# Kernel optimization log

Hardware: AMD Instinct MI355X
Metric: run time of the kernel (lower is better)

## Reference

```python
import jax, jax.numpy as jnp
import numpy as np

EMB, KEY, HEAD, CTX = 1024, 64, 64, 4096
B, T = 4, 4096

def setup_inputs() -> dict:
    key = jax.random.key(0)
    ks = jax.random.split(key, 4)
    s = 1.0 / np.sqrt(EMB)
    return {
        "embeddings": jax.random.normal(ks[0], (B, T, EMB), dtype=jnp.float32),
        "Wk": jax.random.normal(ks[1], (EMB, KEY), dtype=jnp.float32) * s,
        "bk": jnp.zeros((KEY,), dtype=jnp.float32),
        "Wq": jax.random.normal(ks[2], (EMB, KEY), dtype=jnp.float32) * s,
        "bq": jnp.zeros((KEY,), dtype=jnp.float32),
        "Wv": jax.random.normal(ks[3], (EMB, HEAD), dtype=jnp.float32) * s,
        "bv": jnp.zeros((HEAD,), dtype=jnp.float32),
    }

def reference(embeddings, Wk, bk, Wq, bq, Wv, bv):
    # Linear projections: [B, T, E] @ [E, D] -> [B, T, D]
    keys = embeddings @ Wk + bk
    queries = embeddings @ Wq + bq
    values = embeddings @ Wv + bv
    # Scores: [B, T, T]
    scores = jnp.einsum("btd,bsd->bts", queries, keys) / jnp.sqrt(jnp.float32(KEY))
    t = scores.shape[1]
    # causal mask: -inf strictly above diagonal
    causal = jnp.tril(jnp.ones((t, t), dtype=bool))
    scores = jnp.where(causal, scores, -jnp.inf)
    weights = jax.nn.softmax(scores, axis=-1)
    return jnp.einsum("bts,bsh->bth", weights, values)
```

## Files before the change

kernel.cpp:

```cpp
#include <hip/hip_runtime.h>
#include <hip/hip_bf16.h>

#define EMB 1024
#define NB  4
#define TT  4096
#define DD  64

static constexpr float SCALE2 = 0.125f * 1.4426950408889634f;

typedef __bf16          bfrag    __attribute__((ext_vector_type(8)));
typedef float           f32x4    __attribute__((ext_vector_type(4)));
typedef unsigned short  ushort8t __attribute__((ext_vector_type(8)));
typedef unsigned short  ushort4t __attribute__((ext_vector_type(4)));
typedef unsigned int    uint32;
typedef uint32          uint32x4 __attribute__((ext_vector_type(4)));

__device__ __forceinline__ unsigned short f2bf(float f) {
    __hip_bfloat16 h = __float2bfloat16(f);
    return __builtin_bit_cast(unsigned short, h);
}
__device__ __forceinline__ float bf2f(unsigned short u) {
    uint32 v = ((uint32)u) << 16;
    return __builtin_bit_cast(float, v);
}
__device__ __forceinline__ uint32 pk2(float a, float b) {
    return (uint32)f2bf(a) | ((uint32)f2bf(b) << 16);
}

__global__ __launch_bounds__(256) void prep_wt(
    const float* __restrict__ Wk, const float* __restrict__ Wq,
    const float* __restrict__ Wv, unsigned short* __restrict__ Wt)
{
    const int o = blockIdx.x * 256 + threadIdx.x;
    const int n = o >> 10, k = o & 1023;
    float v;
    if (n < 64)       v = Wk[k * 64 + n];
    else if (n < 128) v = Wq[k * 64 + (n - 64)] * SCALE2;
    else              v = Wv[k * 64 + (n - 128)];
    Wt[o] = f2bf(v);
}

#define PSTR 66

__global__ __launch_bounds__(256) void qkv_mfma(
    const float* __restrict__ emb,
    const unsigned short* __restrict__ Wt,
    const float* __restrict__ bk, const float* __restrict__ bq,
    const float* __restrict__ bv,
    unsigned short* __restrict__ Qb, unsigned short* __restrict__ Kb,
    unsigned short* __restrict__ Vt)
{
    __shared__ unsigned short elds[64 * PSTR];
    __shared__ unsigned short wlds[192 * PSTR];

    const int tid = threadIdx.x;
    const int w = tid >> 6, l = tid & 63;
    const int lr = l & 15, lg = l >> 4;
    const int m0 = blockIdx.x * 64;

    f32x4 acc[12];
#pragma unroll
    for (int i = 0; i < 12; ++i) acc[i] = (f32x4){0.f, 0.f, 0.f, 0.f};

    const int er = tid >> 2, ec = (tid & 3) * 16;

    float4 f0, f1, f2, f3;
    ushort8t wr[6];
    {
        const float* src = emb + (size_t)(m0 + er) * EMB + ec;
        f0 = *(const float4*)(src + 0);
        f1 = *(const float4*)(src + 4);
        f2 = *(const float4*)(src + 8);
        f3 = *(const float4*)(src + 12);
#pragma unroll
        for (int i = 0; i < 6; ++i) {
            const int idx = tid + i * 256;
            const int row = idx >> 3, c = (idx & 7) * 8;
            wr[i] = *(const ushort8t*)&Wt[(size_t)row * 1024 + c];
        }
    }

    for (int it = 0; it < 16; ++it) {
        __syncthreads();
        {
            ushort8t lo, hi;
            lo[0]=f2bf(f0.x); lo[1]=f2bf(f0.y); lo[2]=f2bf(f0.z); lo[3]=f2bf(f0.w);
            lo[4]=f2bf(f1.x); lo[5]=f2bf(f1.y); lo[6]=f2bf(f1.z); lo[7]=f2bf(f1.w);
            hi[0]=f2bf(f2.x); hi[1]=f2bf(f2.y); hi[2]=f2bf(f2.z); hi[3]=f2bf(f2.w);
            hi[4]=f2bf(f3.x); hi[5]=f2bf(f3.y); hi[6]=f2bf(f3.z); hi[7]=f2bf(f3.w);
            *(ushort8t*)&elds[er * PSTR + ec]     = lo;
            *(ushort8t*)&elds[er * PSTR + ec + 8] = hi;
#pragma unroll
            for (int i = 0; i < 6; ++i) {
                const int idx = tid + i * 256;
                const int row = idx >> 3, c = (idx & 7) * 8;
                *(ushort8t*)&wlds[row * PSTR + c] = wr[i];
            }
        }
        if (it < 15) {
            const int kn = (it + 1) * 64;
            const float* src = emb + (size_t)(m0 + er) * EMB + kn + ec;
            f0 = *(const float4*)(src + 0);
            f1 = *(const float4*)(src + 4);
            f2 = *(const float4*)(src + 8);
            f3 = *(const float4*)(src + 12);
#pragma unroll
            for (int i = 0; i < 6; ++i) {
                const int idx = tid + i * 256;
                const int row = idx >> 3, c = (idx & 7) * 8;
                wr[i] = *(const ushort8t*)&Wt[(size_t)row * 1024 + kn + c];
            }
        }
        __syncthreads();
#pragma unroll
        for (int c = 0; c < 2; ++c) {
            bfrag a = *(const bfrag*)&elds[(w * 16 + lr) * PSTR + c * 32 + lg * 8];
#pragma unroll
            for (int nt = 0; nt < 12; ++nt) {
                bfrag bb = *(const bfrag*)&wlds[(nt * 16 + lr) * PSTR + c * 32 + lg * 8];
                acc[nt] = __builtin_amdgcn_mfma_f32_16x16x32_bf16(a, bb, acc[nt], 0, 0, 0);
            }
        }
    }

    const int rbase = m0 + w * 16 + lg * 4;
#pragma unroll
    for (int nt = 0; nt < 12; ++nt) {
        const int n = nt * 16 + lr;
        float bias;
        if (n < 64)       bias = bk[n];
        else if (n < 128) bias = bq[n - 64] * SCALE2;
        else              bias = bv[n - 128];
        if (nt < 8) {
            unsigned short* dst = (nt < 4) ? Kb : Qb;
            const int d = (nt < 4) ? n : (n - 64);
#pragma unroll
            for (int rg = 0; rg < 4; ++rg)
                dst[(size_t)(rbase + rg) * 64 + d] = f2bf(acc[nt][rg] + bias);
        } else {
            const int h = n - 128;
            const int b = rbase >> 12, t = rbase & (TT - 1);
            ushort4t pk;
#pragma unroll
            for (int rg = 0; rg < 4; ++rg) pk[rg] = f2bf(acc[nt][rg] + bias);
            *(ushort4t*)&Vt[((size_t)b * 64 + h) * TT + t] = pk;
        }
    }
}

#define LOADK(KF, T)                                                          \
    { const unsigned short* p_ = kp0 + (size_t)(T) * 4096;                    \
      KF[0][0] = *(const bfrag*)(p_);         KF[0][1] = *(const bfrag*)(p_ + 32);   \
      KF[1][0] = *(const bfrag*)(p_ + 1024);  KF[1][1] = *(const bfrag*)(p_ + 1056); \
      KF[2][0] = *(const bfrag*)(p_ + 2048);  KF[2][1] = *(const bfrag*)(p_ + 2080); \
      KF[3][0] = *(const bfrag*)(p_ + 3072);  KF[3][1] = *(const bfrag*)(p_ + 3104); }

#define LOADV(VF, T)                                                          \
    { const unsigned short* p_ = vp0 + (T) * 64;                              \
      VF[0][0] = *(const bfrag*)(p_);             VF[0][1] = *(const bfrag*)(p_ + 32);           \
      VF[1][0] = *(const bfrag*)(p_ + 16 * TT);   VF[1][1] = *(const bfrag*)(p_ + 16 * TT + 32); \
      VF[2][0] = *(const bfrag*)(p_ + 32 * TT);   VF[2][1] = *(const bfrag*)(p_ + 32 * TT + 32); \
      VF[3][0] = *(const bfrag*)(p_ + 48 * TT);   VF[3][1] = *(const bfrag*)(p_ + 48 * TT + 32); }

#define COMPUTE(KF, VF, T)                                                    \
{                                                                             \
    const int  kt_   = kt0 + (T);                                             \
    const bool diag_ = (kt_ == nkt - 1);                                      \
    const int  k0_   = kt_ * 64;                                              \
    _Pragma("unroll")                                                         \
    for (int s = 0; s < 2; ++s) {                                             \
        f32x4 sv[4];                                                          \
        __builtin_amdgcn_s_setprio(1);                                        \
        _Pragma("unroll")                                                     \
        for (int nt = 0; nt < 4; ++nt) {                                      \
            sv[nt] = (f32x4){0.f, 0.f, 0.f, 0.f};                             \
            sv[nt] = __builtin_amdgcn_mfma_f32_16x16x32_bf16(KF[nt][0], qa[s][0], sv[nt], 0, 0, 0); \
            sv[nt] = __builtin_amdgcn_mfma_f32_16x16x32_bf16(KF[nt][1], qa[s][1], sv[nt], 0, 0, 0); \
        }                                                                     \
        __builtin_amdgcn_s_setprio(0);                                        \
        const int qrow_ = q0 + s * 16 + lr;                                   \
        if (diag_) {                                                          \
            _Pragma("unroll")                                                 \
            for (int nt = 0; nt < 4; ++nt)                                    \
                _Pragma("unroll")                                             \
                for (int rg = 0; rg < 4; ++rg) {                              \
                    const int key_ = k0_ + nt * 16 + 4 * g + rg;              \
                    if (key_ > qrow_) sv[nt][rg] = -1e30f;                    \
                }                                                             \
        }                                                                     \
        float pm = fmaxf(fmaxf(fmaxf(sv[0][0], sv[0][1]), fmaxf(sv[0][2], sv[0][3])),   \
                         fmaxf(fmaxf(sv[1][0], sv[1][1]), fmaxf(sv[1][2], sv[1][3])));  \
        pm = fmaxf(pm, fmaxf(fmaxf(fmaxf(sv[2][0], sv[2][1]), fmaxf(sv[2][2], sv[2][3])),   \
                             fmaxf(fmaxf(sv[3][0], sv[3][1]), fmaxf(sv[3][2], sv[3][3])))); \
        pm = fmaxf(pm, __shfl_xor(pm, 16));                                   \
        pm = fmaxf(pm, __shfl_xor(pm, 32));                                   \
        if (!__all(pm - mrow[s] <= 8.0f)) {                                   \
            const float nm_ = fmaxf(mrow[s], pm);                             \
            const float cr_ = exp2f(mrow[s] - nm_);                           \
            mrow[s] = nm_;                                                    \
            lrow[s] *= cr_;                                                   \
            _Pragma("unroll")                                                 \
            for (int ht = 0; ht < 4; ++ht) o[s][ht] *= cr_;                   \
        }                                                                     \
        float ls = 0.f;                                                       \
        uint32 pw[8];                                                         \
        _Pragma("unroll")                                                     \
        for (int nt = 0; nt < 4; ++nt)                                        \
            _Pragma("unroll")                                                 \
            for (int h = 0; h < 2; ++h) {                                     \
                const float pa_ = exp2f(sv[nt][2 * h]     - mrow[s]);         \
                const float pb_ = exp2f(sv[nt][2 * h + 1] - mrow[s]);         \
                ls += pa_ + pb_;                                              \
                pw[nt * 2 + h] = pk2(pa_, pb_);                               \
            }                                                                 \
        ls += __shfl_xor(ls, 16);                                             \
        ls += __shfl_xor(ls, 32);                                             \
        lrow[s] += ls;                                                        \
        _Pragma("unroll")                                                     \
        for (int cc = 0; cc < 2; ++cc) {                                      \
            uint32x4 dw;                                                      \
            _Pragma("unroll")                                                 \
            for (int w2 = 0; w2 < 4; ++w2) {                                  \
                const int addr_ = (w2 < 2) ? addr_a : addr_b;                 \
                const uint32 lo_ = (uint32)__builtin_amdgcn_ds_bpermute(      \
                    addr_, (int)pw[4 * cc + (w2 & 1)]);                       \
                const uint32 hi_ = (uint32)__builtin_amdgcn_ds_bpermute(      \
                    addr_, (int)pw[4 * cc + 2 + (w2 & 1)]);                   \
                dw[w2] = ghi ? hi_ : lo_;                                     \
            }                                                                 \
            const bfrag paf_ = __builtin_bit_cast(bfrag, dw);                 \
            __builtin_amdgcn_s_setprio(1);                                    \
            o[s][0] = __builtin_amdgcn_mfma_f32_16x16x32_bf16(paf_, VF[0][cc], o[s][0], 0, 0, 0); \
            o[s][1] = __builtin_amdgcn_mfma_f32_16x16x32_bf16(paf_, VF[1][cc], o[s][1], 0, 0, 0); \
            o[s][2] = __builtin_amdgcn_mfma_f32_16x16x32_bf16(paf_, VF[2][cc], o[s][2], 0, 0, 0); \
            o[s][3] = __builtin_amdgcn_mfma_f32_16x16x32_bf16(paf_, VF[3][cc], o[s][3], 0, 0, 0); \
            __builtin_amdgcn_s_setprio(0);                                    \
        }                                                                     \
    }                                                                         \
}

template<int CHUNK>
__global__ __launch_bounds__(256, 2) void attn_part(
    const unsigned short* __restrict__ Qb,
    const unsigned short* __restrict__ Kb,
    const unsigned short* __restrict__ Vt,
    unsigned short* __restrict__ po, float* __restrict__ pml)
{
    constexpr int NCH = 64 / CHUNK;
    const int idx   = blockIdx.x;
    const int wid   = threadIdx.x >> 6;
    const int c     = (idx >> 9) * 4 + wid;
    const int layer = idx & 511;
    const int b     = layer & 3;
    const int ti32  = 127 - ((layer >> 2) & 127);
    const int nkt   = (ti32 >> 1) + 1;
    const int kt0   = c * CHUNK;
    if (kt0 >= nkt) return;
    const int ntile = min(nkt - kt0, CHUNK);

    const int l  = threadIdx.x & 63;
    const int lr = l & 15, g = l >> 4;
    const int q0 = ti32 * 32;
    const size_t bTT = (size_t)b * TT;

    bfrag qa[2][2];
#pragma unroll
    for (int s = 0; s < 2; ++s) {
        const size_t qr = (bTT + q0 + s * 16 + lr) * 64 + g * 8;
        qa[s][0] = *(const bfrag*)&Qb[qr];
        qa[s][1] = *(const bfrag*)&Qb[qr + 32];
    }

    const unsigned short* kp0 = Kb + (bTT + (size_t)kt0 * 64 + lr) * 64 + g * 8;
    const unsigned short* vp0 = Vt + ((size_t)b * 64 + lr) * TT + (size_t)kt0 * 64 + g * 8;

    const int addr_a = (lr + 32 * (g & 1)) * 4;
    const int addr_b = addr_a + 64;
    const bool ghi = (g >= 2);

    f32x4 o[2][4];
#pragma unroll
    for (int s = 0; s < 2; ++s)
#pragma unroll
        for (int ht = 0; ht < 4; ++ht) o[s][ht] = (f32x4){0.f, 0.f, 0.f, 0.f};
    float mrow[2] = {-1e30f, -1e30f};
    float lrow[2] = {0.f, 0.f};

    bfrag kfA[4][2], kfB[4][2], vf[4][2];
    LOADK(kfA, 0);

#pragma unroll
    for (int t = 0; t < CHUNK; t += 2) {
        if (t >= ntile) break;
        LOADV(vf, t);
        if (t + 1 < ntile) LOADK(kfB, t + 1);
        COMPUTE(kfA, vf, t);
        if (t + 1 >= ntile) break;
        LOADV(vf, t + 1);
        if (t + 2 < ntile) LOADK(kfA, t + 2);
        COMPUTE(kfB, vf, t + 1);
    }

    const int slot = (((b << 7) + ti32) * NCH) + c;
    const size_t pob = (size_t)slot * 2048;
#pragma unroll
    for (int s = 0; s < 2; ++s)
#pragma unroll
        for (int ht = 0; ht < 4; ++ht)
#pragma unroll
            for (int rg = 0; rg < 4; ++rg)
                po[pob + (size_t)(((s * 4 + ht) * 4 + rg) * 64 + l)] = f2bf(o[s][ht][rg]);
    if (g == 0) {
#pragma unroll
        for (int s = 0; s < 2; ++s) {
            pml[slot * 64 + s * 16 + lr]      = mrow[s];
            pml[slot * 64 + 32 + s * 16 + lr] = lrow[s];
        }
    }
}

__global__ __launch_bounds__(256) void attn_merge(
    const unsigned short* __restrict__ po, const float* __restrict__ pml,
    float* __restrict__ out, int chunk, int nch)
{
    const int idx  = blockIdx.x;
    const int b    = idx & 3;
    const int ti32 = idx >> 2;
    const int nkt  = (ti32 >> 1) + 1;
    const int nc   = (nkt + chunk - 1) / chunk;

    const int e0   = threadIdx.x * 8;
    const int lane = e0 & 63;
    const int rg   = (e0 >> 6) & 3;
    const int ht   = (e0 >> 8) & 3;
    const int s    = e0 >> 10;
    const int row  = s * 16 + ((lane >> 4) << 2) + rg;
    const int col0 = ht * 16 + (lane & 15);
    const int slot0 = ((b << 7) + ti32) * nch;

    float M = -1e30f;
    for (int c = 0; c < nc; ++c)
        M = fmaxf(M, pml[(slot0 + c) * 64 + row]);

    float den = 0.f;
    float acc[8];
#pragma unroll
    for (int i = 0; i < 8; ++i) acc[i] = 0.f;

    for (int c = 0; c < nc; ++c) {
        const float wgt = exp2f(pml[(slot0 + c) * 64 + row] - M);
        den += wgt * pml[(slot0 + c) * 64 + 32 + row];
        const ushort8t v = *(const ushort8t*)&po[(size_t)(slot0 + c) * 2048 + e0];
#pragma unroll
        for (int j = 0; j < 8; ++j) acc[j] += wgt * bf2f(v[j]);
    }
    const float inv = 1.0f / den;
    float* dst = out + ((size_t)b * TT + ti32 * 32 + row) * 64 + col0;
    float4 o0 = {acc[0] * inv, acc[1] * inv, acc[2] * inv, acc[3] * inv};
    float4 o1 = {acc[4] * inv, acc[5] * inv, acc[6] * inv, acc[7] * inv};
    *(float4*)(dst)     = o0;
    *(float4*)(dst + 4) = o1;
}

extern "C" void kernel_launch(void* const* d_in, const int* in_sizes, int n_in,
                              void* d_out, int out_size, void* d_ws, size_t ws_size,
                              hipStream_t stream)
{
    const float* emb = (const float*)d_in[0];
    const float* Wk  = (const float*)d_in[1];
    const float* bk  = (const float*)d_in[2];
    const float* Wq  = (const float*)d_in[3];
    const float* bq  = (const float*)d_in[4];
    const float* Wv  = (const float*)d_in[5];
    const float* bv  = (const float*)d_in[6];
    float* out = (float*)d_out;

    char* base = (char*)d_ws;
    unsigned short* Qb = (unsigned short*)(base);
    unsigned short* Kb = (unsigned short*)(base + (2u << 20));
    unsigned short* Vt = (unsigned short*)(base + (4u << 20));
    unsigned short* Wt = (unsigned short*)(base + (6u << 20));
    const size_t pbase = ((size_t)6 << 20) + (512u << 10);

    int nch = 16;
    {
        const size_t need16 = pbase +
            (size_t)512 * 16 * (2048 * sizeof(unsigned short) + 64 * sizeof(float));
        if (need16 > ws_size) nch = 8;
    }
    const int chunk = 64 / nch;
    unsigned short* po = (unsigned short*)(base + pbase);
    float* pml = (float*)(po + (size_t)512 * nch * 2048);

    prep_wt<<<192 * 1024 / 256, 256, 0, stream>>>(Wk, Wq, Wv, Wt);
    qkv_mfma<<<(NB * TT) / 64, 256, 0, stream>>>(emb, Wt, bk, bq, bv, Qb, Kb, Vt);
    if (nch == 16)
        attn_part<4><<<512 * 4, 256, 0, stream>>>(Qb, Kb, Vt, po, pml);
    else
        attn_part<8><<<512 * 2, 256, 0, stream>>>(Qb, Kb, Vt, po, pml);
    attn_merge<<<512, 256, 0, stream>>>(po, pml, out, chunk, nch);
}
```

Before: 89.29 us.

## Use single-wave attention blocks, split merge, packed bf16 convert and max-tree

Attention partial blocks shrink from four waves to one wave of 64 threads, so each chunk is its own block. This lets the scheduler drop blocks for early-exit chunks independently and balance the causal workload more finely. The merge kernel is split into two blocks per tile, each thread handling 4 elements, to double its parallelism. Separately, the bf16 pair pack uses the v_cvt_pk_bf16_f32 instruction and the row-max reduction is reshaped into two chains. The cost is many more tiny blocks with launch overhead, and launch_bounds(64,2) may change register allocation.

New measurement: 86.00 us. -3.7%, faster.

```diff
diff --git a/kernel.cpp b/kernel.cpp
--- a/kernel.cpp
+++ b/kernel.cpp
@@ -24,7 +24,9 @@
     return __builtin_bit_cast(float, v);
 }
 __device__ __forceinline__ uint32 pk2(float a, float b) {
-    return (uint32)f2bf(a) | ((uint32)f2bf(b) << 16);
+    uint32 r;
+    asm("v_cvt_pk_bf16_f32 %0, %1, %2" : "=v"(r) : "v"(a), "v"(b));
+    return r;
 }
 
 __global__ __launch_bounds__(256) void prep_wt(
@@ -188,10 +190,14 @@
                     if (key_ > qrow_) sv[nt][rg] = -1e30f;                    \
                 }                                                             \
         }                                                                     \
-        float pm = fmaxf(fmaxf(fmaxf(sv[0][0], sv[0][1]), fmaxf(sv[0][2], sv[0][3])),   \
-                         fmaxf(fmaxf(sv[1][0], sv[1][1]), fmaxf(sv[1][2], sv[1][3])));  \
-        pm = fmaxf(pm, fmaxf(fmaxf(fmaxf(sv[2][0], sv[2][1]), fmaxf(sv[2][2], sv[2][3])),   \
-                             fmaxf(fmaxf(sv[3][0], sv[3][1]), fmaxf(sv[3][2], sv[3][3])))); \
+                  \
+        float a0_ = fmaxf(fmaxf(sv[0][0], sv[0][1]), sv[0][2]);               \
+        a0_ = fmaxf(fmaxf(a0_, sv[0][3]), sv[1][0]);                          \
+        a0_ = fmaxf(fmaxf(a0_, sv[1][1]), sv[1][2]);                          \
+        float a1_ = fmaxf(fmaxf(sv[2][0], sv[2][1]), sv[2][2]);               \
+        a1_ = fmaxf(fmaxf(a1_, sv[2][3]), sv[3][0]);                          \
+        a1_ = fmaxf(fmaxf(a1_, sv[3][1]), sv[3][2]);                          \
+        float pm = fmaxf(fmaxf(a0_, sv[1][3]), fmaxf(a1_, sv[3][3]));         \
         pm = fmaxf(pm, __shfl_xor(pm, 16));                                   \
         pm = fmaxf(pm, __shfl_xor(pm, 32));                                   \
         if (!__all(pm - mrow[s] <= 8.0f)) {                                   \
@@ -240,25 +246,23 @@
 }
 
 template<int CHUNK>
-__global__ __launch_bounds__(256, 2) void attn_part(
+__global__ __launch_bounds__(64, 2) void attn_part(
     const unsigned short* __restrict__ Qb,
     const unsigned short* __restrict__ Kb,
     const unsigned short* __restrict__ Vt,
     unsigned short* __restrict__ po, float* __restrict__ pml)
 {
     constexpr int NCH = 64 / CHUNK;
-    const int idx   = blockIdx.x;
-    const int wid   = threadIdx.x >> 6;
-    const int c     = (idx >> 9) * 4 + wid;
-    const int layer = idx & 511;
-    const int b     = layer & 3;
-    const int ti32  = 127 - ((layer >> 2) & 127);
-    const int nkt   = (ti32 >> 1) + 1;
-    const int kt0   = c * CHUNK;
+    const int idx  = blockIdx.x;
+    const int c    = idx >> 9;
+    const int b    = idx & 3;
+    const int ti32 = 127 - ((idx >> 2) & 127);
+    const int nkt  = (ti32 >> 1) + 1;
+    const int kt0  = c * CHUNK;
     if (kt0 >= nkt) return;
     const int ntile = min(nkt - kt0, CHUNK);
 
-    const int l  = threadIdx.x & 63;
+    const int l  = threadIdx.x;
     const int lr = l & 15, g = l >> 4;
     const int q0 = ti32 * 32;
     const size_t bTT = (size_t)b * TT;
@@ -323,13 +327,14 @@
     const unsigned short* __restrict__ po, const float* __restrict__ pml,
     float* __restrict__ out, int chunk, int nch)
 {
-    const int idx  = blockIdx.x;
+    const int idx  = blockIdx.x >> 1;
+    const int half = blockIdx.x & 1;
     const int b    = idx & 3;
     const int ti32 = idx >> 2;
     const int nkt  = (ti32 >> 1) + 1;
     const int nc   = (nkt + chunk - 1) / chunk;
 
-    const int e0   = threadIdx.x * 8;
+    const int e0   = half * 1024 + threadIdx.x * 4;
     const int lane = e0 & 63;
     const int rg   = (e0 >> 6) & 3;
     const int ht   = (e0 >> 8) & 3;
@@ -343,23 +348,21 @@
         M = fmaxf(M, pml[(slot0 + c) * 64 + row]);
 
     float den = 0.f;
-    float acc[8];
-#pragma unroll
-    for (int i = 0; i < 8; ++i) acc[i] = 0.f;
+    float acc[4];
+#pragma unroll
+    for (int i = 0; i < 4; ++i) acc[i] = 0.f;
 
     for (int c = 0; c < nc; ++c) {
         const float wgt = exp2f(pml[(slot0 + c) * 64 + row] - M);
         den += wgt * pml[(slot0 + c) * 64 + 32 + row];
-        const ushort8t v = *(const ushort8t*)&po[(size_t)(slot0 + c) * 2048 + e0];
-#pragma unroll
-        for (int j = 0; j < 8; ++j) acc[j] += wgt * bf2f(v[j]);
+        const ushort4t v = *(const ushort4t*)&po[(size_t)(slot0 + c) * 2048 + e0];
+#pragma unroll
+        for (int j = 0; j < 4; ++j) acc[j] += wgt * bf2f(v[j]);
     }
     const float inv = 1.0f / den;
     float* dst = out + ((size_t)b * TT + ti32 * 32 + row) * 64 + col0;
     float4 o0 = {acc[0] * inv, acc[1] * inv, acc[2] * inv, acc[3] * inv};
-    float4 o1 = {acc[4] * inv, acc[5] * inv, acc[6] * inv, acc[7] * inv};
-    *(float4*)(dst)     = o0;
-    *(float4*)(dst + 4) = o1;
+    *(float4*)(dst) = o0;
 }
 
 extern "C" void kernel_launch(void* const* d_in, const int* in_sizes, int n_in,
@@ -395,8 +398,8 @@
     prep_wt<<<192 * 1024 / 256, 256, 0, stream>>>(Wk, Wq, Wv, Wt);
     qkv_mfma<<<(NB * TT) / 64, 256, 0, stream>>>(emb, Wt, bk, bq, bv, Qb, Kb, Vt);
     if (nch == 16)
-        attn_part<4><<<512 * 4, 256, 0, stream>>>(Qb, Kb, Vt, po, pml);
+        attn_part<4><<<512 * 16, 64, 0, stream>>>(Qb, Kb, Vt, po, pml);
     else
-        attn_part<8><<<512 * 2, 256, 0, stream>>>(Qb, Kb, Vt, po, pml);
-    attn_merge<<<512, 256, 0, stream>>>(po, pml, out, chunk, nch);
-}
+        attn_part<8><<<512 * 8, 64, 0, stream>>>(Qb, Kb, Vt, po, pml);
+    attn_merge<<<1024, 256, 0, stream>>>(po, pml, out, chunk, nch);
+}
```
